# Kernel tuning notes

Measured on AMD Instinct MI355X. Metric: run time of the kernel, lower is better.

The kernel has to match this reference:

```python
import jax, jax.numpy as jnp
import numpy as np

LN_EPS = 1e-5

def setup_inputs() -> dict:
    key = jax.random.key(0)
    ks = jax.random.split(key, 10)
    B, L, D2 = 64, 512, 16  # batch, max_len_text, 2*n_degree
    V, D, C = 8000, 256, 4  # n_word, d_model, n_category
    E = (V - 1) * V + 1      # edge-weight table size
    x = jax.random.randint(ks[0], (B, L), 0, V, dtype=jnp.int32)
    nb_x = jax.random.randint(ks[1], (B, L, D2), 0, V, dtype=jnp.int32)
    w_edge = jax.random.randint(ks[2], (B, L, D2), 0, E, dtype=jnp.int32)
    emb_weight = jax.random.normal(ks[3], (V, D), jnp.float32) * 0.02
    emb_weight = emb_weight.at[0].set(0.0)  # padding_idx=0
    w_edge_table = jax.random.normal(ks[4], (E, 1), jnp.float32) * 0.02
    w_edge_table = w_edge_table.at[0].set(0.0)
    eta_table = jax.random.normal(ks[5], (V, 1), jnp.float32) * 0.02
    eta_table = eta_table.at[0].set(0.0)
    ln_gamma = jnp.ones((D,), jnp.float32)
    ln_beta = jnp.zeros((D,), jnp.float32)
    fc_w = jax.random.normal(ks[6], (D, C), jnp.float32) * 0.02
    fc_b = jnp.zeros((C,), jnp.float32)
    return {"x": x, "nb_x": nb_x, "w_edge": w_edge,
            "emb_weight": emb_weight, "w_edge_table": w_edge_table,
            "eta_table": eta_table, "ln_gamma": ln_gamma, "ln_beta": ln_beta,
            "fc_w": fc_w, "fc_b": fc_b}

def _layernorm(h, gamma, beta):
    mu = jnp.mean(h, axis=-1, keepdims=True)
    var = jnp.mean(jnp.square(h - mu), axis=-1, keepdims=True)
    return (h - mu) * jax.lax.rsqrt(var + LN_EPS) * gamma + beta

def reference(x, nb_x, w_edge, emb_weight, w_edge_table, eta_table,
              ln_gamma, ln_beta, fc_w, fc_b):
    # idx_nodes: (B, L, 2*deg + 1) -- neighbors then self
    idx_nodes = jnp.concatenate([nb_x, x[..., None]], axis=-1)
    emb_nodes = emb_weight[idx_nodes]                  # (B, L, 2d+1, D)
    emb_nodes = _layernorm(emb_nodes, ln_gamma, ln_beta)
    we = w_edge_table[w_edge]                          # (B, L, 2d, 1)
    msg_nb = jnp.max(we * emb_nodes[:, :, :-1, :], axis=2)  # (B, L, D)
    eta = eta_table[x]                                 # (B, L, 1)
    h_node = (1.0 - eta) * msg_nb + eta * emb_nodes[:, :, -1, :]
    scores = h_node.sum(axis=1) @ fc_w + fc_b          # (B, C)
    return scores
```

## Files before the change

kernel.cpp:

```cpp
#include <hip/hip_runtime.h>
#include <math.h>

#define DV   256
#define BB   64
#define LL   512
#define DEG2 16
#define VV   8000
#define CC   4
#define LSPLIT 64
#define LN_EPS 1e-5f

typedef _Float16 half4 __attribute__((ext_vector_type(4)));
typedef float    f32x4 __attribute__((ext_vector_type(4)));

__global__ void __launch_bounds__(64) ln_rows_kernel(
    const float* __restrict__ emb, const float* __restrict__ gamma,
    const float* __restrict__ beta, half4* __restrict__ out)
{
    const int row = blockIdx.x;
    const int ln  = threadIdx.x;

    const f32x4 v = ((const f32x4*)(emb + row * DV))[ln];

    float s = v[0] + v[1] + v[2] + v[3];
    #pragma unroll
    for (int off = 32; off > 0; off >>= 1) s += __shfl_xor(s, off);
    const float mu = s * (1.0f / DV);

    f32x4 c;
    #pragma unroll
    for (int k = 0; k < 4; ++k) c[k] = v[k] - mu;

    float q = c[0]*c[0] + c[1]*c[1] + c[2]*c[2] + c[3]*c[3];
    #pragma unroll
    for (int off = 32; off > 0; off >>= 1) q += __shfl_xor(q, off);
    const float rs = rsqrtf(q * (1.0f / DV) + LN_EPS);

    const f32x4 g = ((const f32x4*)gamma)[ln];
    const f32x4 bt = ((const f32x4*)beta)[ln];

    half4 h;
    #pragma unroll
    for (int k = 0; k < 4; ++k) h[k] = (_Float16)(c[k] * rs * g[k] + bt[k]);
    out[row * 64 + ln] = h;
}

__global__ void __launch_bounds__(256) gather_kernel(
    const int* __restrict__ w_edge, const float* __restrict__ we_table,
    const int* __restrict__ x,      const float* __restrict__ eta_table,
    float* __restrict__ we_flat,    float* __restrict__ eta_flat)
{
    const int i = blockIdx.x * 256 + threadIdx.x;
    we_flat[i] = we_table[w_edge[i]];
    if (i < BB * LL) eta_flat[i] = eta_table[x[i]];
}

__global__ void __launch_bounds__(256) gnn_kernel(
    const int*   __restrict__ nb_x,
    const int*   __restrict__ x,
    const float* __restrict__ we_flat,
    const float* __restrict__ eta_flat,
    const half4* __restrict__ norm_emb,
    float*       __restrict__ h_part)
{
    const int b   = blockIdx.x;
    const int lc  = blockIdx.y;
    const int w   = __builtin_amdgcn_readfirstlane(threadIdx.x >> 6);
    const int ln  = threadIdx.x & 63;

    f32x4 acc = {0.0f, 0.0f, 0.0f, 0.0f};

    #pragma unroll
    for (int li = 0; li < 2; ++li) {
        const int l    = lc * 8 + w * 2 + li;
        const int base = b * LL + l;

        const int*   nb  = nb_x    + base * DEG2;
        const float* wep = we_flat + base * DEG2;

        f32x4 m = {-INFINITY, -INFINITY, -INFINITY, -INFINITY};
        #pragma unroll
        for (int j = 0; j < DEG2; ++j) {
            const int   idx = nb[j];
            const float wej = wep[j];
            const half4 e = norm_emb[idx * 64 + ln];
            #pragma unroll
            for (int k = 0; k < 4; ++k)
                m[k] = fmaxf(m[k], wej * (float)e[k]);
        }

        const int   sidx = x[base];
        const float eta  = eta_flat[base];
        const half4 se   = norm_emb[sidx * 64 + ln];
        #pragma unroll
        for (int k = 0; k < 4; ++k)
            acc[k] += (1.0f - eta) * m[k] + eta * (float)se[k];
    }

    __shared__ float s_acc[4][DV];
    ((f32x4*)s_acc[w])[ln] = acc;
    __syncthreads();
    if (w == 0) {
        f32x4 r0 = ((f32x4*)s_acc[0])[ln];
        f32x4 r1 = ((f32x4*)s_acc[1])[ln];
        f32x4 r2 = ((f32x4*)s_acc[2])[ln];
        f32x4 r3 = ((f32x4*)s_acc[3])[ln];
        f32x4 r;
        #pragma unroll
        for (int k = 0; k < 4; ++k) r[k] = r0[k] + r1[k] + r2[k] + r3[k];
        ((f32x4*)(h_part + (b * LSPLIT + lc) * DV))[ln] = r;
    }
}

__global__ void __launch_bounds__(256) fc_kernel(
    const float* __restrict__ h_part,
    const float* __restrict__ fc_w,
    const float* __restrict__ fc_b,
    float*       __restrict__ out)
{
    const int b  = blockIdx.x;
    const int d  = threadIdx.x;
    const int w  = d >> 6;
    const int ln = d & 63;

    float h = 0.0f;
    #pragma unroll 8
    for (int lc = 0; lc < LSPLIT; ++lc)
        h += h_part[(b * LSPLIT + lc) * DV + d];

    float p[CC];
    #pragma unroll
    for (int c = 0; c < CC; ++c) p[c] = h * fc_w[d * CC + c];

    #pragma unroll
    for (int c = 0; c < CC; ++c)
        #pragma unroll
        for (int off = 32; off > 0; off >>= 1) p[c] += __shfl_xor(p[c], off);

    __shared__ float s_red[4][CC];
    if (ln == 0) {
        #pragma unroll
        for (int c = 0; c < CC; ++c) s_red[w][c] = p[c];
    }
    __syncthreads();
    if (d < CC)
        out[b * CC + d] = s_red[0][d] + s_red[1][d] + s_red[2][d] + s_red[3][d] + fc_b[d];
}

extern "C" void kernel_launch(void* const* d_in, const int* in_sizes, int n_in,
                              void* d_out, int out_size, void* d_ws, size_t ws_size,
                              hipStream_t stream) {
    const int*   x        = (const int*)  d_in[0];
    const int*   nb_x     = (const int*)  d_in[1];
    const int*   w_edge   = (const int*)  d_in[2];
    const float* emb_w    = (const float*)d_in[3];
    const float* we_table = (const float*)d_in[4];
    const float* eta_tab  = (const float*)d_in[5];
    const float* ln_gamma = (const float*)d_in[6];
    const float* ln_beta  = (const float*)d_in[7];
    const float* fc_w     = (const float*)d_in[8];
    const float* fc_b     = (const float*)d_in[9];
    float* out = (float*)d_out;

    char* ws = (char*)d_ws;
    half4* norm_emb = (half4*)(ws);
    float* we_flat  = (float*)(ws + 4096000);
    float* eta_flat = (float*)(ws + 4096000 + 2097152);
    float* h_part   = (float*)(ws + 4096000 + 2097152 + 131072);

    ln_rows_kernel<<<VV, 64, 0, stream>>>(emb_w, ln_gamma, ln_beta, norm_emb);

    gather_kernel<<<(BB * LL * DEG2) / 256, 256, 0, stream>>>(
        w_edge, we_table, x, eta_tab, we_flat, eta_flat);

    dim3 grid3(BB, LSPLIT);
    gnn_kernel<<<grid3, 256, 0, stream>>>(nb_x, x, we_flat, eta_flat, norm_emb, h_part);

    fc_kernel<<<BB, 256, 0, stream>>>(h_part, fc_w, fc_b, out);
}
```

Baseline: 48.23 us.

## Fuse edge-weight and eta gathers into GNN kernel via LDS staging

Removes the separate gather kernel that wrote we_flat and eta_flat to global memory. The GNN kernel now loads the neighbor indices and edge-table lookups cooperatively, one lane per edge, and stages them in shared memory as int2 pairs. Each wave now processes 4 positions instead of 2, which halves the grid along L. This drops one launch and a write-then-read round trip through global memory, at the cost of an extra barrier and fewer blocks in flight.

```diff
diff --git a/kernel.cpp b/kernel.cpp
--- a/kernel.cpp
+++ b/kernel.cpp
@@ -7,7 +7,10 @@
 #define DEG2 16
 #define VV   8000
 #define CC   4
-#define LSPLIT 64
+#define LPW  4
+#define NW   4
+#define LCB  (LPW*NW)
+#define NLC  (LL/LCB)
 #define LN_EPS 1e-5f
 
 typedef _Float16 half4 __attribute__((ext_vector_type(4)));
@@ -36,7 +39,7 @@
     for (int off = 32; off > 0; off >>= 1) q += __shfl_xor(q, off);
     const float rs = rsqrtf(q * (1.0f / DV) + LN_EPS);
 
-    const f32x4 g = ((const f32x4*)gamma)[ln];
+    const f32x4 g  = ((const f32x4*)gamma)[ln];
     const f32x4 bt = ((const f32x4*)beta)[ln];
 
     half4 h;
@@ -45,59 +48,64 @@
     out[row * 64 + ln] = h;
 }
 
-__global__ void __launch_bounds__(256) gather_kernel(
-    const int* __restrict__ w_edge, const float* __restrict__ we_table,
-    const int* __restrict__ x,      const float* __restrict__ eta_table,
-    float* __restrict__ we_flat,    float* __restrict__ eta_flat)
-{
-    const int i = blockIdx.x * 256 + threadIdx.x;
-    we_flat[i] = we_table[w_edge[i]];
-    if (i < BB * LL) eta_flat[i] = eta_table[x[i]];
-}
-
 __global__ void __launch_bounds__(256) gnn_kernel(
     const int*   __restrict__ nb_x,
+    const int*   __restrict__ w_edge,
+    const float* __restrict__ we_table,
     const int*   __restrict__ x,
-    const float* __restrict__ we_flat,
-    const float* __restrict__ eta_flat,
+    const float* __restrict__ eta_table,
     const half4* __restrict__ norm_emb,
     float*       __restrict__ h_part)
 {
     const int b   = blockIdx.x;
     const int lc  = blockIdx.y;
-    const int w   = __builtin_amdgcn_readfirstlane(threadIdx.x >> 6);
-    const int ln  = threadIdx.x & 63;
+    const int tid = threadIdx.x;
+    const int w   = tid >> 6;
+    const int ln  = tid & 63;
+
+    const int l0   = lc * LCB + w * LPW;
+    const int base = b * LL + l0;
+
+    const int   nbv = nb_x  [base * DEG2 + ln];
+    const int   eiv = w_edge[base * DEG2 + ln];
+    const float wev = we_table[eiv];
+
+    int   xv = 0; float etv = 0.0f;
+    if (ln < LPW) { xv = x[base + ln]; etv = eta_table[xv]; }
+
+    __shared__ int2  s_pair[NW][64];
+    __shared__ int   s_self[NW][LPW];
+    __shared__ float s_eta [NW][LPW];
+
+    int2 pr; pr.x = nbv; pr.y = __float_as_int(wev);
+    s_pair[w][ln] = pr;
+    if (ln < LPW) { s_self[w][ln] = xv; s_eta[w][ln] = etv; }
+    __syncthreads();
 
     f32x4 acc = {0.0f, 0.0f, 0.0f, 0.0f};
 
     #pragma unroll
-    for (int li = 0; li < 2; ++li) {
-        const int l    = lc * 8 + w * 2 + li;
-        const int base = b * LL + l;
-
-        const int*   nb  = nb_x    + base * DEG2;
-        const float* wep = we_flat + base * DEG2;
-
+    for (int li = 0; li < LPW; ++li) {
         f32x4 m = {-INFINITY, -INFINITY, -INFINITY, -INFINITY};
         #pragma unroll
         for (int j = 0; j < DEG2; ++j) {
-            const int   idx = nb[j];
-            const float wej = wep[j];
-            const half4 e = norm_emb[idx * 64 + ln];
+            const int2  p   = s_pair[w][li * DEG2 + j];
+            const int   idx = p.x;
+            const float wej = __int_as_float(p.y);
+            const half4 e   = norm_emb[idx * 64 + ln];
             #pragma unroll
             for (int k = 0; k < 4; ++k)
                 m[k] = fmaxf(m[k], wej * (float)e[k]);
         }
-
-        const int   sidx = x[base];
-        const float eta  = eta_flat[base];
+        const int   sidx = s_self[w][li];
+        const float eta  = s_eta [w][li];
         const half4 se   = norm_emb[sidx * 64 + ln];
         #pragma unroll
         for (int k = 0; k < 4; ++k)
             acc[k] += (1.0f - eta) * m[k] + eta * (float)se[k];
     }
 
-    __shared__ float s_acc[4][DV];
+    __shared__ float s_acc[NW][DV];
     ((f32x4*)s_acc[w])[ln] = acc;
     __syncthreads();
     if (w == 0) {
@@ -108,7 +116,7 @@
         f32x4 r;
         #pragma unroll
         for (int k = 0; k < 4; ++k) r[k] = r0[k] + r1[k] + r2[k] + r3[k];
-        ((f32x4*)(h_part + (b * LSPLIT + lc) * DV))[ln] = r;
+        ((f32x4*)(h_part + (b * NLC + lc) * DV))[ln] = r;
     }
 }
 
@@ -125,8 +133,8 @@
 
     float h = 0.0f;
     #pragma unroll 8
-    for (int lc = 0; lc < LSPLIT; ++lc)
-        h += h_part[(b * LSPLIT + lc) * DV + d];
+    for (int lc = 0; lc < NLC; ++lc)
+        h += h_part[(b * NLC + lc) * DV + d];
 
     float p[CC];
     #pragma unroll
@@ -164,17 +172,13 @@
 
     char* ws = (char*)d_ws;
     half4* norm_emb = (half4*)(ws);
-    float* we_flat  = (float*)(ws + 4096000);
-    float* eta_flat = (float*)(ws + 4096000 + 2097152);
-    float* h_part   = (float*)(ws + 4096000 + 2097152 + 131072);
+    float* h_part   = (float*)(ws + 4096000);
 
     ln_rows_kernel<<<VV, 64, 0, stream>>>(emb_w, ln_gamma, ln_beta, norm_emb);
 
-    gather_kernel<<<(BB * LL * DEG2) / 256, 256, 0, stream>>>(
-        w_edge, we_table, x, eta_tab, we_flat, eta_flat);
-
-    dim3 grid3(BB, LSPLIT);
-    gnn_kernel<<<grid3, 256, 0, stream>>>(nb_x, x, we_flat, eta_flat, norm_emb, h_part);
+    dim3 grid2(BB, NLC);
+    gnn_kernel<<<grid2, 256, 0, stream>>>(nb_x, w_edge, we_table, x, eta_tab,
+                                          norm_emb, h_part);
 
     fc_kernel<<<BB, 256, 0, stream>>>(h_part, fc_w, fc_b, out);
 }
```

Result: faster. 44.55 us (-7.6%).
